# Performance work log

Hardware: AMD Instinct MI355X
Metric: run time of the kernel (lower is better)

Reference implementation:

```python
import jax, jax.numpy as jnp
import numpy as np

EPS = 1e-09


def make_spd(x):
    # x: [B1, B2, n, n] random normal -> SPD via Gram matrix + jitter
    n = x.shape[-1]
    g = jnp.einsum('...ik,...jk->...ij', x, x) / n
    return g + 1e-3 * jnp.eye(n, dtype=x.dtype)


def setup_inputs() -> dict:
    key = jax.random.key(0)
    x = jax.random.normal(key, (256, 32, 64, 64), dtype=jnp.float32)
    return {"inputs": make_spd(x)}


def reference(inputs) -> jnp.ndarray:
    # Batched matrix log of SPD matrices: V @ diag(log(relu(w)+eps)) @ V^T
    eigval, eigvecs = jnp.linalg.eigh(inputs)            # [..., n], [..., n, n]
    log_s = jnp.log(jax.nn.relu(eigval) + EPS)           # [..., n]
    # fused reconstruction: (V * log_s) @ V^T
    return jnp.einsum('...ij,...j,...kj->...ik', eigvecs, log_s, eigvecs)
```

## Files before the change

kernel.cpp:

```cpp
#include <hip/hip_runtime.h>
#include <math.h>

#define NDIM 64
#define PITCH 68
#define KC 16
#define MAXSWEEPS 20

typedef float v2f __attribute__((ext_vector_type(2)));

__device__ __forceinline__ v2f pk_fma(v2f a, v2f b, v2f c)
{
    v2f d;
    asm("v_pk_fma_f32 %0, %1, %2, %3" : "=v"(d) : "v"(a), "v"(b), "v"(c));
    return d;
}

__device__ __forceinline__ v2f pk_mul(v2f a, v2f b)
{
    v2f d;
    asm("v_pk_mul_f32 %0, %1, %2" : "=v"(d) : "v"(a), "v"(b));
    return d;
}

__global__ __launch_bounds__(64, 3)
void logeig_jacobi_kernel(const float* __restrict__ in, float* __restrict__ out)
{
    const int b    = blockIdx.x;
    const int lane = threadIdx.x;
    const float* A = in  + (size_t)b * (NDIM * NDIM);
    float*       O = out + (size_t)b * (NDIM * NDIM);

    __shared__ float ldsM[KC * PITCH];
    __shared__ float ldsW[NDIM];

    v2f x2[NDIM / 2];
#pragma unroll
    for (int i = 0; i < NDIM / 2; ++i) {
        x2[i].x = A[(2 * i + 0) * NDIM + lane];
        x2[i].y = A[(2 * i + 1) * NDIM + lane];
    }

    float alpha = 0.0f;

#pragma unroll 1
    for (int sweep = 0; sweep < MAXSWEEPS; ++sweep) {
        v2f r0 = {0.f, 0.f}, r1 = {0.f, 0.f};
#pragma unroll
        for (int i = 0; i < NDIM / 2; i += 2) {
            r0 = pk_fma(x2[i],     x2[i],     r0);
            r1 = pk_fma(x2[i + 1], x2[i + 1], r1);
        }
        alpha = (r0.x + r0.y) + (r1.x + r1.y);

        bool any_big = false;
#pragma unroll 1
        for (int mi = 1; mi < NDIM; ++mi) {
            const int m    = (sweep & 1) ? (NDIM - mi) : mi;
            const int pidx = (lane ^ m) << 2;

            v2f y2[NDIM / 2];
#pragma unroll
            for (int i = 0; i < NDIM / 2; ++i) {
                y2[i].x = __int_as_float(__builtin_amdgcn_ds_bpermute(pidx, __float_as_int(x2[i].x)));
                y2[i].y = __int_as_float(__builtin_amdgcn_ds_bpermute(pidx, __float_as_int(x2[i].y)));
            }

            v2f g0 = {0.f, 0.f}, g1 = {0.f, 0.f};
#pragma unroll
            for (int i = 0; i < NDIM / 2; i += 2) {
                g0 = pk_fma(x2[i],     y2[i],     g0);
                g1 = pk_fma(x2[i + 1], y2[i + 1], g1);
            }
            const float gamma = (g0.x + g0.y) + (g1.x + g1.y);

            const float other = __int_as_float(__builtin_amdgcn_ds_bpermute(pidx, __float_as_int(alpha)));

            const bool  is_p = lane < (lane ^ m);
            const float aa = is_p ? alpha : other;
            const float bb = is_p ? other : alpha;

            any_big = any_big || ((gamma * gamma) > (1e-9f * aa * bb));

            const bool  rot = (gamma != 0.0f);
            const float w   = 2.0f * gamma;
            const float d   = bb - aa;
            const float den = fabsf(d) + __builtin_amdgcn_sqrtf(fmaf(w, w, fmaf(d, d, 1e-35f)));
            const float t   = ((d >= 0.0f) ? w : -w) * __builtin_amdgcn_rcpf(den);
            const float cc  = __builtin_amdgcn_rsqf(fmaf(t, t, 1.0f));
            const float ss  = t * cc;

            const float sgn = is_p ? -1.0f : 1.0f;
            const float c_r = rot ? cc : 1.0f;
            const float s_r = rot ? sgn * ss : 0.0f;
            const float tg  = rot ? sgn * t * gamma : 0.0f;

            v2f c2; c2.x = c_r; c2.y = c_r;
            v2f s2; s2.x = s_r; s2.y = s_r;
#pragma unroll
            for (int i = 0; i < NDIM / 2; ++i)
                x2[i] = pk_fma(c2, x2[i], pk_mul(s2, y2[i]));
            alpha += tg;
        }
        if (__ballot(any_big) == 0ull) break;
    }

    v2f f0 = {0.f, 0.f}, f1 = {0.f, 0.f};
#pragma unroll
    for (int i = 0; i < NDIM / 2; i += 2) {
        f0 = pk_fma(x2[i],     x2[i],     f0);
        f1 = pk_fma(x2[i + 1], x2[i + 1], f1);
    }
    const float af  = (f0.x + f0.y) + (f1.x + f1.y);
    const float lam = __builtin_amdgcn_sqrtf(af);
    ldsW[lane] = logf(lam + 1e-9f) / af;

    v2f acc2[NDIM / 2];
#pragma unroll
    for (int i = 0; i < NDIM / 2; ++i) { acc2[i].x = 0.f; acc2[i].y = 0.f; }

#pragma unroll 1
    for (int c = 0; c < NDIM; c += KC) {
        __syncthreads();
        if (lane >= c && lane < c + KC) {
            float4* row = (float4*)&ldsM[(lane - c) * PITCH];
#pragma unroll
            for (int t4 = 0; t4 < NDIM / 4; ++t4)
                row[t4] = make_float4(x2[2 * t4].x, x2[2 * t4].y,
                                      x2[2 * t4 + 1].x, x2[2 * t4 + 1].y);
        }
        __syncthreads();
#pragma unroll 1
        for (int kk = 0; kk < KC; ++kk) {
            const float wk  = ldsW[c + kk];
            const float mlk = ldsM[kk * PITCH + lane];
            const float zk  = wk * mlk;
            v2f zk2; zk2.x = zk; zk2.y = zk;
            const float4* rowk = (const float4*)&ldsM[kk * PITCH];
#pragma unroll
            for (int t4 = 0; t4 < NDIM / 4; ++t4) {
                const float4 v = rowk[t4];
                v2f lo; lo.x = v.x; lo.y = v.y;
                v2f hi; hi.x = v.z; hi.y = v.w;
                acc2[2 * t4]     = pk_fma(zk2, lo, acc2[2 * t4]);
                acc2[2 * t4 + 1] = pk_fma(zk2, hi, acc2[2 * t4 + 1]);
            }
        }
    }

#pragma unroll
    for (int i = 0; i < NDIM / 2; ++i) {
        O[(2 * i + 0) * NDIM + lane] = acc2[i].x;
        O[(2 * i + 1) * NDIM + lane] = acc2[i].y;
    }
}

extern "C" void kernel_launch(void* const* d_in, const int* in_sizes, int n_in,
                              void* d_out, int out_size, void* d_ws, size_t ws_size,
                              hipStream_t stream)
{
    const float* in  = (const float*)d_in[0];
    float*       out = (float*)d_out;
    const int nmat = out_size / (NDIM * NDIM);
    hipLaunchKernelGGL(logeig_jacobi_kernel, dim3(nmat), dim3(64), 0, stream, in, out);
}
```

Before: 5.348 ms.

## Software-pipeline Jacobi partner exchange with rotation and drop single-wave barriers

Restructures the inner Jacobi sweep so the cross-lane bpermute fetch of the next partner column is issued inside the same loop that applies the current rotation. The first exchange is peeled before the loop and the last rotation after it, so the exchange latency can hide behind the packed FMAs. It also uses four dot-product accumulators instead of two, relaxes launch bounds to allow more registers per wave, and removes the __syncthreads around the LDS reconstruction, since each block is a single 64-lane wavefront. The costs are higher register pressure and reliance on in-order LDS access within one wave for correctness.

```diff
diff --git a/kernel.cpp b/kernel.cpp
--- a/kernel.cpp
+++ b/kernel.cpp
@@ -22,7 +22,42 @@
     return d;
 }
 
-__global__ __launch_bounds__(64, 3)
+__device__ __forceinline__ float bpermf(int pidx, float v)
+{
+    return __int_as_float(__builtin_amdgcn_ds_bpermute(pidx, __float_as_int(v)));
+}
+
+#define DOT_SCHUR(MVAL)                                                          \
+    v2f g0 = {0.f,0.f}, g1 = {0.f,0.f}, g2 = {0.f,0.f}, g3 = {0.f,0.f};          \
+    _Pragma("unroll")                                                            \
+    for (int i = 0; i < NDIM / 2; i += 4) {                                      \
+        g0 = pk_fma(x2[i + 0], y2[i + 0], g0);                                   \
+        g1 = pk_fma(x2[i + 1], y2[i + 1], g1);                                   \
+        g2 = pk_fma(x2[i + 2], y2[i + 2], g2);                                   \
+        g3 = pk_fma(x2[i + 3], y2[i + 3], g3);                                   \
+    }                                                                            \
+    const float gamma = ((g0.x + g0.y) + (g1.x + g1.y))                          \
+                      + ((g2.x + g2.y) + (g3.x + g3.y));                         \
+    const bool  is_p = lane < (lane ^ (MVAL));                                   \
+    const float aa = is_p ? alpha : aex;                                         \
+    const float bb = is_p ? aex : alpha;                                         \
+    any_big = any_big || ((gamma * gamma) > (1e-9f * aa * bb));                  \
+    const bool  rot = (gamma != 0.0f);                                           \
+    const float w   = 2.0f * gamma;                                              \
+    const float d   = bb - aa;                                                   \
+    const float den = fabsf(d) + __builtin_amdgcn_sqrtf(fmaf(w, w, fmaf(d, d, 1e-35f))); \
+    const float t   = ((d >= 0.0f) ? w : -w) * __builtin_amdgcn_rcpf(den);       \
+    const float cc  = __builtin_amdgcn_rsqf(fmaf(t, t, 1.0f));                   \
+    const float ss  = t * cc;                                                    \
+    const float sgn = is_p ? -1.0f : 1.0f;                                       \
+    const float c_r = rot ? cc : 1.0f;                                           \
+    const float s_r = rot ? sgn * ss : 0.0f;                                     \
+    const float tg  = rot ? sgn * t * gamma : 0.0f;                              \
+    v2f c2; c2.x = c_r; c2.y = c_r;                                              \
+    v2f s2; s2.x = s_r; s2.y = s_r;                                              \
+    alpha += tg;
+
+__global__ __launch_bounds__(64, 1)
 void logeig_jacobi_kernel(const float* __restrict__ in, float* __restrict__ out)
 {
     const int b    = blockIdx.x;
@@ -52,55 +87,47 @@
         }
         alpha = (r0.x + r0.y) + (r1.x + r1.y);
 
+        const int dir = sweep & 1;
+
+        const int m1    = dir ? (NDIM - 1) : 1;
+        const int pidx1 = (lane ^ m1) << 2;
+        v2f y2[NDIM / 2];
+#pragma unroll
+        for (int i = 0; i < NDIM / 2; ++i) {
+            y2[i].x = bpermf(pidx1, x2[i].x);
+            y2[i].y = bpermf(pidx1, x2[i].y);
+        }
+        float aex = bpermf(pidx1, alpha);
+
         bool any_big = false;
+
 #pragma unroll 1
-        for (int mi = 1; mi < NDIM; ++mi) {
-            const int m    = (sweep & 1) ? (NDIM - mi) : mi;
-            const int pidx = (lane ^ m) << 2;
+        for (int mi = 1; mi < NDIM - 1; ++mi) {
+            const int m      = dir ? (NDIM - mi) : mi;
+            const int m_nx   = dir ? (NDIM - mi - 1) : (mi + 1);
+            const int pidx_n = (lane ^ m_nx) << 2;
 
-            v2f y2[NDIM / 2];
+            DOT_SCHUR(m)
+
+            const float aexn = bpermf(pidx_n, alpha);
+
 #pragma unroll
             for (int i = 0; i < NDIM / 2; ++i) {
-                y2[i].x = __int_as_float(__builtin_amdgcn_ds_bpermute(pidx, __float_as_int(x2[i].x)));
-                y2[i].y = __int_as_float(__builtin_amdgcn_ds_bpermute(pidx, __float_as_int(x2[i].y)));
+                x2[i]   = pk_fma(c2, x2[i], pk_mul(s2, y2[i]));
+                y2[i].x = bpermf(pidx_n, x2[i].x);
+                y2[i].y = bpermf(pidx_n, x2[i].y);
             }
+            aex = aexn;
+        }
 
-            v2f g0 = {0.f, 0.f}, g1 = {0.f, 0.f};
-#pragma unroll
-            for (int i = 0; i < NDIM / 2; i += 2) {
-                g0 = pk_fma(x2[i],     y2[i],     g0);
-                g1 = pk_fma(x2[i + 1], y2[i + 1], g1);
-            }
-            const float gamma = (g0.x + g0.y) + (g1.x + g1.y);
-
-            const float other = __int_as_float(__builtin_amdgcn_ds_bpermute(pidx, __float_as_int(alpha)));
-
-            const bool  is_p = lane < (lane ^ m);
-            const float aa = is_p ? alpha : other;
-            const float bb = is_p ? other : alpha;
-
-            any_big = any_big || ((gamma * gamma) > (1e-9f * aa * bb));
-
-            const bool  rot = (gamma != 0.0f);
-            const float w   = 2.0f * gamma;
-            const float d   = bb - aa;
-            const float den = fabsf(d) + __builtin_amdgcn_sqrtf(fmaf(w, w, fmaf(d, d, 1e-35f)));
-            const float t   = ((d >= 0.0f) ? w : -w) * __builtin_amdgcn_rcpf(den);
-            const float cc  = __builtin_amdgcn_rsqf(fmaf(t, t, 1.0f));
-            const float ss  = t * cc;
-
-            const float sgn = is_p ? -1.0f : 1.0f;
-            const float c_r = rot ? cc : 1.0f;
-            const float s_r = rot ? sgn * ss : 0.0f;
-            const float tg  = rot ? sgn * t * gamma : 0.0f;
-
-            v2f c2; c2.x = c_r; c2.y = c_r;
-            v2f s2; s2.x = s_r; s2.y = s_r;
+        {
+            const int m = dir ? 1 : (NDIM - 1);
+            DOT_SCHUR(m)
 #pragma unroll
             for (int i = 0; i < NDIM / 2; ++i)
                 x2[i] = pk_fma(c2, x2[i], pk_mul(s2, y2[i]));
-            alpha += tg;
         }
+
         if (__ballot(any_big) == 0ull) break;
     }
 
@@ -120,7 +147,6 @@
 
 #pragma unroll 1
     for (int c = 0; c < NDIM; c += KC) {
-        __syncthreads();
         if (lane >= c && lane < c + KC) {
             float4* row = (float4*)&ldsM[(lane - c) * PITCH];
 #pragma unroll
@@ -128,7 +154,6 @@
                 row[t4] = make_float4(x2[2 * t4].x, x2[2 * t4].y,
                                       x2[2 * t4 + 1].x, x2[2 * t4 + 1].y);
         }
-        __syncthreads();
 #pragma unroll 1
         for (int kk = 0; kk < KC; ++kk) {
             const float wk  = ldsW[c + kk];
```

Result: no change. 5.268 ms (-1.5%).

## Process two matrices per wavefront with interleaved Jacobi rotations

Applied to the files above, without the earlier changes.

Each 64-lane block now diagonalizes two SPD matrices at once, interleaving their bpermute exchanges, dot products and rotation updates to expose more independent instructions. The intent is to hide bpermute and dependency latency with instruction-level parallelism instead of relying on several waves per SIMD. The cost is roughly double the register footprint, launch bounds lowered to one wave per SIMD, and sweeps continuing until both matrices converge. The __syncthreads calls around the LDS reconstruction staging are removed, relying on single-wave execution for ordering.

```diff
diff --git a/kernel.cpp b/kernel.cpp
--- a/kernel.cpp
+++ b/kernel.cpp
@@ -22,35 +22,105 @@
     return d;
 }
 
-__global__ __launch_bounds__(64, 3)
+__device__ __forceinline__ float bpermf(int pidx, float v)
+{
+    return __int_as_float(__builtin_amdgcn_ds_bpermute(pidx, __float_as_int(v)));
+}
+
+#define SCHUR(GAMMA, ALPHA, AEX, ISP, C2, S2, TG)                                \
+    {                                                                            \
+        const float aa  = (ISP) ? (ALPHA) : (AEX);                               \
+        const float bb  = (ISP) ? (AEX) : (ALPHA);                               \
+        any_big = any_big || ((GAMMA) * (GAMMA) > (1e-9f * aa * bb));            \
+        const bool  rot = ((GAMMA) != 0.0f);                                     \
+        const float w   = 2.0f * (GAMMA);                                        \
+        const float d   = bb - aa;                                               \
+        const float den = fabsf(d) + __builtin_amdgcn_sqrtf(fmaf(w, w, fmaf(d, d, 1e-35f))); \
+        const float t   = ((d >= 0.0f) ? w : -w) * __builtin_amdgcn_rcpf(den);   \
+        const float cc  = __builtin_amdgcn_rsqf(fmaf(t, t, 1.0f));               \
+        const float ss  = t * cc;                                                \
+        const float sgn = (ISP) ? -1.0f : 1.0f;                                  \
+        const float c_r = rot ? cc : 1.0f;                                       \
+        const float s_r = rot ? sgn * ss : 0.0f;                                 \
+        (TG) = rot ? sgn * t * (GAMMA) : 0.0f;                                   \
+        (C2).x = c_r; (C2).y = c_r;                                              \
+        (S2).x = s_r; (S2).y = s_r;                                              \
+    }
+
+#define RECON(X2, OPTR)                                                          \
+    {                                                                            \
+        v2f acc2[NDIM / 2];                                                      \
+        _Pragma("unroll")                                                        \
+        for (int i = 0; i < NDIM / 2; ++i) { acc2[i].x = 0.f; acc2[i].y = 0.f; } \
+        _Pragma("unroll 1")                                                      \
+        for (int c = 0; c < NDIM; c += KC) {                                     \
+            if (lane >= c && lane < c + KC) {                                    \
+                float4* row = (float4*)&ldsM[(lane - c) * PITCH];                \
+                _Pragma("unroll")                                                \
+                for (int t4 = 0; t4 < NDIM / 4; ++t4)                            \
+                    row[t4] = make_float4(X2[2 * t4].x, X2[2 * t4].y,            \
+                                          X2[2 * t4 + 1].x, X2[2 * t4 + 1].y);   \
+            }                                                                    \
+            _Pragma("unroll 1")                                                  \
+            for (int kk = 0; kk < KC; ++kk) {                                    \
+                const float wk  = ldsW[c + kk];                                  \
+                const float mlk = ldsM[kk * PITCH + lane];                       \
+                const float zk  = wk * mlk;                                      \
+                v2f zk2; zk2.x = zk; zk2.y = zk;                                 \
+                const float4* rowk = (const float4*)&ldsM[kk * PITCH];           \
+                _Pragma("unroll")                                                \
+                for (int t4 = 0; t4 < NDIM / 4; ++t4) {                          \
+                    const float4 v = rowk[t4];                                   \
+                    v2f lo; lo.x = v.x; lo.y = v.y;                              \
+                    v2f hi; hi.x = v.z; hi.y = v.w;                              \
+                    acc2[2 * t4]     = pk_fma(zk2, lo, acc2[2 * t4]);            \
+                    acc2[2 * t4 + 1] = pk_fma(zk2, hi, acc2[2 * t4 + 1]);        \
+                }                                                                \
+            }                                                                    \
+        }                                                                        \
+        _Pragma("unroll")                                                        \
+        for (int i = 0; i < NDIM / 2; ++i) {                                     \
+            (OPTR)[(2 * i + 0) * NDIM + lane] = acc2[i].x;                       \
+            (OPTR)[(2 * i + 1) * NDIM + lane] = acc2[i].y;                       \
+        }                                                                        \
+    }
+
+__global__ __launch_bounds__(64, 1)
 void logeig_jacobi_kernel(const float* __restrict__ in, float* __restrict__ out)
 {
-    const int b    = blockIdx.x;
     const int lane = threadIdx.x;
-    const float* A = in  + (size_t)b * (NDIM * NDIM);
-    float*       O = out + (size_t)b * (NDIM * NDIM);
+    const int b0   = blockIdx.x * 2;
+    const float* A0 = in  + (size_t)b0 * (NDIM * NDIM);
+    const float* A1 = A0 + NDIM * NDIM;
+    float*       O0 = out + (size_t)b0 * (NDIM * NDIM);
+    float*       O1 = O0 + NDIM * NDIM;
 
     __shared__ float ldsM[KC * PITCH];
     __shared__ float ldsW[NDIM];
 
-    v2f x2[NDIM / 2];
+    v2f xa[NDIM / 2], xb[NDIM / 2];
 #pragma unroll
     for (int i = 0; i < NDIM / 2; ++i) {
-        x2[i].x = A[(2 * i + 0) * NDIM + lane];
-        x2[i].y = A[(2 * i + 1) * NDIM + lane];
+        xa[i].x = A0[(2 * i + 0) * NDIM + lane];
+        xa[i].y = A0[(2 * i + 1) * NDIM + lane];
+        xb[i].x = A1[(2 * i + 0) * NDIM + lane];
+        xb[i].y = A1[(2 * i + 1) * NDIM + lane];
     }
 
-    float alpha = 0.0f;
+    float alA = 0.0f, alB = 0.0f;
 
 #pragma unroll 1
     for (int sweep = 0; sweep < MAXSWEEPS; ++sweep) {
-        v2f r0 = {0.f, 0.f}, r1 = {0.f, 0.f};
+        v2f ra0 = {0.f, 0.f}, ra1 = {0.f, 0.f}, rb0 = {0.f, 0.f}, rb1 = {0.f, 0.f};
 #pragma unroll
         for (int i = 0; i < NDIM / 2; i += 2) {
-            r0 = pk_fma(x2[i],     x2[i],     r0);
-            r1 = pk_fma(x2[i + 1], x2[i + 1], r1);
+            ra0 = pk_fma(xa[i],     xa[i],     ra0);
+            ra1 = pk_fma(xa[i + 1], xa[i + 1], ra1);
+            rb0 = pk_fma(xb[i],     xb[i],     rb0);
+            rb1 = pk_fma(xb[i + 1], xb[i + 1], rb1);
         }
-        alpha = (r0.x + r0.y) + (r1.x + r1.y);
+        alA = (ra0.x + ra0.y) + (ra1.x + ra1.y);
+        alB = (rb0.x + rb0.y) + (rb1.x + rb1.y);
 
         bool any_big = false;
 #pragma unroll 1
@@ -58,100 +128,62 @@
             const int m    = (sweep & 1) ? (NDIM - mi) : mi;
             const int pidx = (lane ^ m) << 2;
 
-            v2f y2[NDIM / 2];
+            v2f ya[NDIM / 2], yb[NDIM / 2];
 #pragma unroll
             for (int i = 0; i < NDIM / 2; ++i) {
-                y2[i].x = __int_as_float(__builtin_amdgcn_ds_bpermute(pidx, __float_as_int(x2[i].x)));
-                y2[i].y = __int_as_float(__builtin_amdgcn_ds_bpermute(pidx, __float_as_int(x2[i].y)));
+                ya[i].x = bpermf(pidx, xa[i].x);
+                ya[i].y = bpermf(pidx, xa[i].y);
+                yb[i].x = bpermf(pidx, xb[i].x);
+                yb[i].y = bpermf(pidx, xb[i].y);
             }
 
-            v2f g0 = {0.f, 0.f}, g1 = {0.f, 0.f};
+            v2f ga0 = {0.f, 0.f}, ga1 = {0.f, 0.f}, gb0 = {0.f, 0.f}, gb1 = {0.f, 0.f};
 #pragma unroll
             for (int i = 0; i < NDIM / 2; i += 2) {
-                g0 = pk_fma(x2[i],     y2[i],     g0);
-                g1 = pk_fma(x2[i + 1], y2[i + 1], g1);
+                ga0 = pk_fma(xa[i],     ya[i],     ga0);
+                ga1 = pk_fma(xa[i + 1], ya[i + 1], ga1);
+                gb0 = pk_fma(xb[i],     yb[i],     gb0);
+                gb1 = pk_fma(xb[i + 1], yb[i + 1], gb1);
             }
-            const float gamma = (g0.x + g0.y) + (g1.x + g1.y);
+            const float gammaA = (ga0.x + ga0.y) + (ga1.x + ga1.y);
+            const float gammaB = (gb0.x + gb0.y) + (gb1.x + gb1.y);
 
-            const float other = __int_as_float(__builtin_amdgcn_ds_bpermute(pidx, __float_as_int(alpha)));
+            const float aexA = bpermf(pidx, alA);
+            const float aexB = bpermf(pidx, alB);
+            const bool  is_p = lane < (lane ^ m);
 
-            const bool  is_p = lane < (lane ^ m);
-            const float aa = is_p ? alpha : other;
-            const float bb = is_p ? other : alpha;
+            v2f c2a, s2a, c2b, s2b;
+            float tgA, tgB;
+            SCHUR(gammaA, alA, aexA, is_p, c2a, s2a, tgA)
+            SCHUR(gammaB, alB, aexB, is_p, c2b, s2b, tgB)
 
-            any_big = any_big || ((gamma * gamma) > (1e-9f * aa * bb));
-
-            const bool  rot = (gamma != 0.0f);
-            const float w   = 2.0f * gamma;
-            const float d   = bb - aa;
-            const float den = fabsf(d) + __builtin_amdgcn_sqrtf(fmaf(w, w, fmaf(d, d, 1e-35f)));
-            const float t   = ((d >= 0.0f) ? w : -w) * __builtin_amdgcn_rcpf(den);
-            const float cc  = __builtin_amdgcn_rsqf(fmaf(t, t, 1.0f));
-            const float ss  = t * cc;
-
-            const float sgn = is_p ? -1.0f : 1.0f;
-            const float c_r = rot ? cc : 1.0f;
-            const float s_r = rot ? sgn * ss : 0.0f;
-            const float tg  = rot ? sgn * t * gamma : 0.0f;
-
-            v2f c2; c2.x = c_r; c2.y = c_r;
-            v2f s2; s2.x = s_r; s2.y = s_r;
 #pragma unroll
-            for (int i = 0; i < NDIM / 2; ++i)
-                x2[i] = pk_fma(c2, x2[i], pk_mul(s2, y2[i]));
-            alpha += tg;
+            for (int i = 0; i < NDIM / 2; ++i) {
+                xa[i] = pk_fma(c2a, xa[i], pk_mul(s2a, ya[i]));
+                xb[i] = pk_fma(c2b, xb[i], pk_mul(s2b, yb[i]));
+            }
+            alA += tgA;
+            alB += tgB;
         }
         if (__ballot(any_big) == 0ull) break;
     }
 
-    v2f f0 = {0.f, 0.f}, f1 = {0.f, 0.f};
+    v2f fa0 = {0.f, 0.f}, fa1 = {0.f, 0.f}, fb0 = {0.f, 0.f}, fb1 = {0.f, 0.f};
 #pragma unroll
     for (int i = 0; i < NDIM / 2; i += 2) {
-        f0 = pk_fma(x2[i],     x2[i],     f0);
-        f1 = pk_fma(x2[i + 1], x2[i + 1], f1);
+        fa0 = pk_fma(xa[i],     xa[i],     fa0);
+        fa1 = pk_fma(xa[i + 1], xa[i + 1], fa1);
+        fb0 = pk_fma(xb[i],     xb[i],     fb0);
+        fb1 = pk_fma(xb[i + 1], xb[i + 1], fb1);
     }
-    const float af  = (f0.x + f0.y) + (f1.x + f1.y);
-    const float lam = __builtin_amdgcn_sqrtf(af);
-    ldsW[lane] = logf(lam + 1e-9f) / af;
+    const float afA = (fa0.x + fa0.y) + (fa1.x + fa1.y);
+    const float afB = (fb0.x + fb0.y) + (fb1.x + fb1.y);
 
-    v2f acc2[NDIM / 2];
-#pragma unroll
-    for (int i = 0; i < NDIM / 2; ++i) { acc2[i].x = 0.f; acc2[i].y = 0.f; }
+    ldsW[lane] = logf(__builtin_amdgcn_sqrtf(afA) + 1e-9f) / afA;
+    RECON(xa, O0)
 
-#pragma unroll 1
-    for (int c = 0; c < NDIM; c += KC) {
-        __syncthreads();
-        if (lane >= c && lane < c + KC) {
-            float4* row = (float4*)&ldsM[(lane - c) * PITCH];
-#pragma unroll
-            for (int t4 = 0; t4 < NDIM / 4; ++t4)
-                row[t4] = make_float4(x2[2 * t4].x, x2[2 * t4].y,
-                                      x2[2 * t4 + 1].x, x2[2 * t4 + 1].y);
-        }
-        __syncthreads();
-#pragma unroll 1
-        for (int kk = 0; kk < KC; ++kk) {
-            const float wk  = ldsW[c + kk];
-            const float mlk = ldsM[kk * PITCH + lane];
-            const float zk  = wk * mlk;
-            v2f zk2; zk2.x = zk; zk2.y = zk;
-            const float4* rowk = (const float4*)&ldsM[kk * PITCH];
-#pragma unroll
-            for (int t4 = 0; t4 < NDIM / 4; ++t4) {
-                const float4 v = rowk[t4];
-                v2f lo; lo.x = v.x; lo.y = v.y;
-                v2f hi; hi.x = v.z; hi.y = v.w;
-                acc2[2 * t4]     = pk_fma(zk2, lo, acc2[2 * t4]);
-                acc2[2 * t4 + 1] = pk_fma(zk2, hi, acc2[2 * t4 + 1]);
-            }
-        }
-    }
-
-#pragma unroll
-    for (int i = 0; i < NDIM / 2; ++i) {
-        O[(2 * i + 0) * NDIM + lane] = acc2[i].x;
-        O[(2 * i + 1) * NDIM + lane] = acc2[i].y;
-    }
+    ldsW[lane] = logf(__builtin_amdgcn_sqrtf(afB) + 1e-9f) / afB;
+    RECON(xb, O1)
 }
 
 extern "C" void kernel_launch(void* const* d_in, const int* in_sizes, int n_in,
@@ -161,5 +193,5 @@
     const float* in  = (const float*)d_in[0];
     float*       out = (float*)d_out;
     const int nmat = out_size / (NDIM * NDIM);
-    hipLaunchKernelGGL(logeig_jacobi_kernel, dim3(nmat), dim3(64), 0, stream, in, out);
+    hipLaunchKernelGGL(logeig_jacobi_kernel, dim3(nmat / 2), dim3(64), 0, stream, in, out);
 }
```

Measured after the change: 7.256 ms. 35.7% more time.

## Split each Jacobi matrix across two wavefronts with LDS-reduced dot products

Applied to the files above, without the earlier changes.

Each 64x64 matrix is now processed by a 128-thread block, with each wavefront holding 32 of the rows. The column-pair dot products and norms become partial sums combined through double-buffered shared memory with a block barrier on every rotation step. The intent is to halve each wave's register footprint and per-step permute/FMA work, giving more parallelism per matrix. In exchange it adds a __syncthreads and LDS round trip to every one of the 63 rotation steps per sweep.

```diff
diff --git a/kernel.cpp b/kernel.cpp
--- a/kernel.cpp
+++ b/kernel.cpp
@@ -2,8 +2,8 @@
 #include <math.h>
 
 #define NDIM 64
-#define PITCH 68
-#define KC 16
+#define NV   16
+#define KC   16
 #define MAXSWEEPS 20
 
 typedef float v2f __attribute__((ext_vector_type(2)));
@@ -22,22 +22,31 @@
     return d;
 }
 
-__global__ __launch_bounds__(64, 3)
+__device__ __forceinline__ float bpermf(int pidx, float v)
+{
+    return __int_as_float(__builtin_amdgcn_ds_bpermute(pidx, __float_as_int(v)));
+}
+
+__global__ __launch_bounds__(128, 3)
 void logeig_jacobi_kernel(const float* __restrict__ in, float* __restrict__ out)
 {
-    const int b    = blockIdx.x;
-    const int lane = threadIdx.x;
-    const float* A = in  + (size_t)b * (NDIM * NDIM);
-    float*       O = out + (size_t)b * (NDIM * NDIM);
+    const int tid   = threadIdx.x;
+    const int h     = tid >> 6;
+    const int lane  = tid & 63;
+    const int rbase = h << 5;
+    const int b     = blockIdx.x;
+    const float* A  = in  + (size_t)b * (NDIM * NDIM);
+    float*       O  = out + (size_t)b * (NDIM * NDIM);
 
-    __shared__ float ldsM[KC * PITCH];
+    __shared__ float ldsG[2][2 * NDIM];
     __shared__ float ldsW[NDIM];
+    __shared__ float ldsM[KC][68];
 
-    v2f x2[NDIM / 2];
+    v2f x2[NV];
 #pragma unroll
-    for (int i = 0; i < NDIM / 2; ++i) {
-        x2[i].x = A[(2 * i + 0) * NDIM + lane];
-        x2[i].y = A[(2 * i + 1) * NDIM + lane];
+    for (int i = 0; i < NV; ++i) {
+        x2[i].x = A[(rbase + 2 * i + 0) * NDIM + lane];
+        x2[i].y = A[(rbase + 2 * i + 1) * NDIM + lane];
     }
 
     float alpha = 0.0f;
@@ -46,11 +55,13 @@
     for (int sweep = 0; sweep < MAXSWEEPS; ++sweep) {
         v2f r0 = {0.f, 0.f}, r1 = {0.f, 0.f};
 #pragma unroll
-        for (int i = 0; i < NDIM / 2; i += 2) {
+        for (int i = 0; i < NV; i += 2) {
             r0 = pk_fma(x2[i],     x2[i],     r0);
             r1 = pk_fma(x2[i + 1], x2[i + 1], r1);
         }
-        alpha = (r0.x + r0.y) + (r1.x + r1.y);
+        ldsG[0][(h << 6) + lane] = (r0.x + r0.y) + (r1.x + r1.y);
+        __syncthreads();
+        alpha = ldsG[0][lane] + ldsG[0][NDIM + lane];
 
         bool any_big = false;
 #pragma unroll 1
@@ -58,26 +69,30 @@
             const int m    = (sweep & 1) ? (NDIM - mi) : mi;
             const int pidx = (lane ^ m) << 2;
 
-            v2f y2[NDIM / 2];
+            v2f y2[NV];
 #pragma unroll
-            for (int i = 0; i < NDIM / 2; ++i) {
-                y2[i].x = __int_as_float(__builtin_amdgcn_ds_bpermute(pidx, __float_as_int(x2[i].x)));
-                y2[i].y = __int_as_float(__builtin_amdgcn_ds_bpermute(pidx, __float_as_int(x2[i].y)));
+            for (int i = 0; i < NV; ++i) {
+                y2[i].x = bpermf(pidx, x2[i].x);
+                y2[i].y = bpermf(pidx, x2[i].y);
             }
 
             v2f g0 = {0.f, 0.f}, g1 = {0.f, 0.f};
 #pragma unroll
-            for (int i = 0; i < NDIM / 2; i += 2) {
+            for (int i = 0; i < NV; i += 2) {
                 g0 = pk_fma(x2[i],     y2[i],     g0);
                 g1 = pk_fma(x2[i + 1], y2[i + 1], g1);
             }
-            const float gamma = (g0.x + g0.y) + (g1.x + g1.y);
+            const float gh = (g0.x + g0.y) + (g1.x + g1.y);
 
-            const float other = __int_as_float(__builtin_amdgcn_ds_bpermute(pidx, __float_as_int(alpha)));
+            const float aex = bpermf(pidx, alpha);
+
+            ldsG[mi & 1][(h << 6) + lane] = gh;
+            __syncthreads();
+            const float gamma = ldsG[mi & 1][lane] + ldsG[mi & 1][NDIM + lane];
 
             const bool  is_p = lane < (lane ^ m);
-            const float aa = is_p ? alpha : other;
-            const float bb = is_p ? other : alpha;
+            const float aa = is_p ? alpha : aex;
+            const float bb = is_p ? aex : alpha;
 
             any_big = any_big || ((gamma * gamma) > (1e-9f * aa * bb));
 
@@ -97,7 +112,7 @@
             v2f c2; c2.x = c_r; c2.y = c_r;
             v2f s2; s2.x = s_r; s2.y = s_r;
 #pragma unroll
-            for (int i = 0; i < NDIM / 2; ++i)
+            for (int i = 0; i < NV; ++i)
                 x2[i] = pk_fma(c2, x2[i], pk_mul(s2, y2[i]));
             alpha += tg;
         }
@@ -106,38 +121,40 @@
 
     v2f f0 = {0.f, 0.f}, f1 = {0.f, 0.f};
 #pragma unroll
-    for (int i = 0; i < NDIM / 2; i += 2) {
+    for (int i = 0; i < NV; i += 2) {
         f0 = pk_fma(x2[i],     x2[i],     f0);
         f1 = pk_fma(x2[i + 1], x2[i + 1], f1);
     }
-    const float af  = (f0.x + f0.y) + (f1.x + f1.y);
-    const float lam = __builtin_amdgcn_sqrtf(af);
-    ldsW[lane] = logf(lam + 1e-9f) / af;
+    ldsG[0][(h << 6) + lane] = (f0.x + f0.y) + (f1.x + f1.y);
+    __syncthreads();
+    const float af = ldsG[0][lane] + ldsG[0][NDIM + lane];
+    if (h == 0)
+        ldsW[lane] = logf(__builtin_amdgcn_sqrtf(af) + 1e-9f) / af;
 
-    v2f acc2[NDIM / 2];
+    v2f acc2[NV];
 #pragma unroll
-    for (int i = 0; i < NDIM / 2; ++i) { acc2[i].x = 0.f; acc2[i].y = 0.f; }
+    for (int i = 0; i < NV; ++i) { acc2[i].x = 0.f; acc2[i].y = 0.f; }
 
 #pragma unroll 1
     for (int c = 0; c < NDIM; c += KC) {
         __syncthreads();
         if (lane >= c && lane < c + KC) {
-            float4* row = (float4*)&ldsM[(lane - c) * PITCH];
+            float4* rowp = (float4*)&ldsM[lane - c][rbase];
 #pragma unroll
-            for (int t4 = 0; t4 < NDIM / 4; ++t4)
-                row[t4] = make_float4(x2[2 * t4].x, x2[2 * t4].y,
-                                      x2[2 * t4 + 1].x, x2[2 * t4 + 1].y);
+            for (int t4 = 0; t4 < 8; ++t4)
+                rowp[t4] = make_float4(x2[2 * t4].x, x2[2 * t4].y,
+                                       x2[2 * t4 + 1].x, x2[2 * t4 + 1].y);
         }
         __syncthreads();
 #pragma unroll 1
         for (int kk = 0; kk < KC; ++kk) {
             const float wk  = ldsW[c + kk];
-            const float mlk = ldsM[kk * PITCH + lane];
+            const float mlk = ldsM[kk][lane];
             const float zk  = wk * mlk;
             v2f zk2; zk2.x = zk; zk2.y = zk;
-            const float4* rowk = (const float4*)&ldsM[kk * PITCH];
+            const float4* rowk = (const float4*)&ldsM[kk][rbase];
 #pragma unroll
-            for (int t4 = 0; t4 < NDIM / 4; ++t4) {
+            for (int t4 = 0; t4 < 8; ++t4) {
                 const float4 v = rowk[t4];
                 v2f lo; lo.x = v.x; lo.y = v.y;
                 v2f hi; hi.x = v.z; hi.y = v.w;
@@ -148,9 +165,9 @@
     }
 
 #pragma unroll
-    for (int i = 0; i < NDIM / 2; ++i) {
-        O[(2 * i + 0) * NDIM + lane] = acc2[i].x;
-        O[(2 * i + 1) * NDIM + lane] = acc2[i].y;
+    for (int i = 0; i < NV; ++i) {
+        O[(rbase + 2 * i + 0) * NDIM + lane] = acc2[i].x;
+        O[(rbase + 2 * i + 1) * NDIM + lane] = acc2[i].y;
     }
 }
 
@@ -161,5 +178,5 @@
     const float* in  = (const float*)d_in[0];
     float*       out = (float*)d_out;
     const int nmat = out_size / (NDIM * NDIM);
-    hipLaunchKernelGGL(logeig_jacobi_kernel, dim3(nmat), dim3(64), 0, stream, in, out);
+    hipLaunchKernelGGL(logeig_jacobi_kernel, dim3(nmat), dim3(128), 0, stream, in, out);
 }
```

Measured after the change: 5.721 ms. 7.0% more time.
